# Kernel optimization log

Hardware: AMD Instinct MI355X
Metric: run time of the kernel (lower is better)

## Reference

```python
import jax, jax.numpy as jnp
import numpy as np

# TT-matrix embedding: vocab = 50*60*60 = 180000, embed_dim = 8*8*8 = 512, tt_rank = 16
M1, M2, M3 = 50, 60, 60        # row modes (index factorization)
N1, N2, N3 = 8, 8, 8           # col modes (embedding-dim factorization)
R = 16                         # TT rank
SENT, BATCH = 2048, 64
VOCAB = M1 * M2 * M3


def setup_inputs() -> dict:
    key = jax.random.key(0)
    k1, k2, k3, kx = jax.random.split(key, 4)
    scale = 0.3  # per-core stddev (t3.random_matrix uses a similar per-core normal init)
    # core k stored with the gathered (row-mode) axis first so gather is a plain take
    core1 = jax.random.normal(k1, (M1, N1, R), dtype=jnp.float32) * scale       # [m1, n1, r]
    core2 = jax.random.normal(k2, (M2, R, N2, R), dtype=jnp.float32) * scale    # [m2, r, n2, r]
    core3 = jax.random.normal(k3, (M3, R, N3), dtype=jnp.float32) * scale       # [m3, r, n3]
    x = jax.random.randint(kx, (SENT, BATCH), 0, VOCAB, dtype=jnp.int64)        # batch_dim_last=True layout
    return {"x": x, "core1": core1, "core2": core2, "core3": core3}


def reference(x, core1, core2, core3):
    # batch_dim_last=True: x is [sent, batch] -> permute to [batch, sent]
    sent, batch = x.shape
    flat = x.T.reshape(-1)                      # [T] flat token ids, T = batch*sent
    # t3.ind2sub: row-major mixed-radix decomposition over row modes [M1, M2, M3]
    i1 = flat // (M2 * M3)
    rem = flat % (M2 * M3)
    i2 = rem // M3
    i3 = rem % M3
    # gather one slice per TT core
    g1 = core1[i1]                              # [T, n1, r]
    g2 = core2[i2]                              # [T, r, n2, r]
    g3 = core3[i3]                              # [T, r, n3]
    # contract cores -> full embedding rows (t3.gather_rows(...).full())
    t12 = jnp.einsum('tar,trbs->tabs', g1, g2)  # [T, n1, n2, r]
    emb = jnp.einsum('tabs,tsc->tabc', t12, g3) # [T, n1, n2, n3]
    rows = emb.reshape(batch, sent, N1 * N2 * N3)
    # batch_dim_last=True: permute back to [sent, batch, emb_dim]
    return rows.transpose(1, 0, 2)
```

## Files before the change

kernel.cpp:

```cpp
#include <hip/hip_runtime.h>


#define M2M3 3600u
#define M3   60u
#define NPAIR 3000
#define CHUNK 16

__global__ __launch_bounds__(256) void tt_pair_kernel(
    const float* __restrict__ c1,
    const float* __restrict__ c2,
    float* __restrict__ tab)
{
    const int pair = blockIdx.x;
    const int i1 = pair / 60;
    const int i2 = pair - i1 * 60;
    const int tid = threadIdx.x;
    const int q  = tid >> 6;
    const int ab = tid & 63;
    const int a  = ab >> 3;
    const int b  = ab & 7;

    const float* __restrict__ g1 = c1 + i1 * 128 + a * 16;
    const float* __restrict__ g2 = c2 + i2 * 2048 + b * 16 + q * 4;

    float4 acc = make_float4(0.f, 0.f, 0.f, 0.f);
#pragma unroll
    for (int r = 0; r < 16; ++r) {
        const float a1 = g1[r];
        const float4 v = *(const float4*)(g2 + r * 128);
        acc.x = fmaf(a1, v.x, acc.x);
        acc.y = fmaf(a1, v.y, acc.y);
        acc.z = fmaf(a1, v.z, acc.z);
        acc.w = fmaf(a1, v.w, acc.w);
    }
    *(float4*)(tab + (size_t)pair * 1024 + tid * 4) = acc;
}

__global__ __launch_bounds__(256) void tt_zero_counts(unsigned* __restrict__ counts)
{
    const int i = blockIdx.x * blockDim.x + threadIdx.x;
    if (i < NPAIR) counts[i] = 0u;
}

__global__ __launch_bounds__(256) void tt_hist(
    const int* __restrict__ x, unsigned* __restrict__ counts, int T)
{
    const int t = blockIdx.x * blockDim.x + threadIdx.x;
    if (t >= T) return;
    const unsigned id = (unsigned)x[t];
    atomicAdd(&counts[id / M3], 1u);
}

__global__ __launch_bounds__(1024) void tt_scan(
    const unsigned* __restrict__ counts, unsigned* __restrict__ cursor)
{
    __shared__ unsigned buf[1024];
    const int tid = threadIdx.x;
    const int b = tid * 3;
    unsigned c0 = 0, c1 = 0, c2 = 0;
    if (b     < NPAIR) c0 = counts[b];
    if (b + 1 < NPAIR) c1 = counts[b + 1];
    if (b + 2 < NPAIR) c2 = counts[b + 2];
    const unsigned local = c0 + c1 + c2;
    buf[tid] = local;
    __syncthreads();
    for (int off = 1; off < 1024; off <<= 1) {
        const unsigned v = (tid >= off) ? buf[tid - off] : 0u;
        __syncthreads();
        buf[tid] += v;
        __syncthreads();
    }
    const unsigned excl = buf[tid] - local;
    if (b     < NPAIR) cursor[b]     = excl;
    if (b + 1 < NPAIR) cursor[b + 1] = excl + c0;
    if (b + 2 < NPAIR) cursor[b + 2] = excl + c0 + c1;
}

__global__ __launch_bounds__(256) void tt_scatter(
    const int* __restrict__ x, unsigned* __restrict__ cursor,
    unsigned* __restrict__ recT, unsigned* __restrict__ recPI, int T)
{
    const int t = blockIdx.x * blockDim.x + threadIdx.x;
    if (t >= T) return;
    const unsigned id   = (unsigned)x[t];
    const unsigned pair = id / M3;
    const unsigned i3   = id - pair * M3;
    const unsigned pos  = atomicAdd(&cursor[pair], 1u);
    recT[pos]  = (unsigned)t;
    recPI[pos] = (pair << 6) | i3;
}

__global__ __launch_bounds__(256) void tt_embed_sorted(
    const unsigned* __restrict__ recT,
    const unsigned* __restrict__ recPI,
    const float* __restrict__ c3,
    const float* __restrict__ tab,
    float* __restrict__ out,
    int T)
{
    const int wid  = (int)((blockIdx.x * blockDim.x + threadIdx.x) >> 6);
    const int lane = threadIdx.x & 63;
    const int base = wid * CHUNK;
    if (base >= T) return;

    unsigned rT = 0u, rP = 0u;
    if (lane < CHUNK && base + lane < T) {
        rT = recT[base + lane];
        rP = recPI[base + lane];
    }

    const int n = min(CHUNK, T - base);
    float4 t4[4];
    int cur = -1;

    for (int j = 0; j < n; ++j) {
        const unsigned tt = __builtin_amdgcn_readlane(rT, j);
        const unsigned pi = __builtin_amdgcn_readlane(rP, j);
        const int      pair = (int)(pi >> 6);
        const unsigned i3   = pi & 63u;

        if (pair != cur) {
            cur = pair;
            const float* tp = tab + (size_t)pair * 1024u;
#pragma unroll
            for (int q = 0; q < 4; ++q)
                t4[q] = *(const float4*)(tp + q * 256 + lane * 4);
        }
        const float* tf = (const float*)t4;

        const float4* __restrict__ g3 = (const float4*)(c3 + i3 * 128u);

        float o[8];
#pragma unroll
        for (int c = 0; c < 8; ++c) o[c] = 0.f;
#pragma unroll
        for (int s = 0; s < 16; ++s) {
            const float ts = tf[s];
            const float4 w0 = g3[s * 2 + 0];
            const float4 w1 = g3[s * 2 + 1];
            o[0] = fmaf(ts, w0.x, o[0]);
            o[1] = fmaf(ts, w0.y, o[1]);
            o[2] = fmaf(ts, w0.z, o[2]);
            o[3] = fmaf(ts, w0.w, o[3]);
            o[4] = fmaf(ts, w1.x, o[4]);
            o[5] = fmaf(ts, w1.y, o[5]);
            o[6] = fmaf(ts, w1.z, o[6]);
            o[7] = fmaf(ts, w1.w, o[7]);
        }

        float4* dst = (float4*)(out + (size_t)tt * 512u + lane * 8);
        dst[0] = make_float4(o[0], o[1], o[2], o[3]);
        dst[1] = make_float4(o[4], o[5], o[6], o[7]);
    }
}

__global__ __launch_bounds__(256) void tt_embed2_kernel(
    const int* __restrict__ x, const float* __restrict__ c3,
    const float* __restrict__ tab, float* __restrict__ out, int T)
{
    const int u    = (int)((blockIdx.x * blockDim.x + threadIdx.x) >> 6);
    const int lane = threadIdx.x & 63;
    if (u >= T) return;
    const unsigned id  = __builtin_amdgcn_readfirstlane((unsigned)x[u]);
    const unsigned i1  = id / M2M3;
    const unsigned rem = id - i1 * M2M3;
    const unsigned i2  = rem / M3;
    const unsigned i3  = rem - i2 * M3;
    const float* tp = tab + (size_t)(i1 * 60u + i2) * 1024u;
    float4 t[4];
#pragma unroll
    for (int q = 0; q < 4; ++q)
        t[q] = *(const float4*)(tp + q * 256 + lane * 4);
    const float* tf = (const float*)t;
    const float4* __restrict__ g3 = (const float4*)(c3 + i3 * 128u);
    float o[8];
#pragma unroll
    for (int c = 0; c < 8; ++c) o[c] = 0.f;
#pragma unroll
    for (int s = 0; s < 16; ++s) {
        const float ts = tf[s];
        const float4 w0 = g3[s * 2 + 0];
        const float4 w1 = g3[s * 2 + 1];
        o[0]=fmaf(ts,w0.x,o[0]); o[1]=fmaf(ts,w0.y,o[1]);
        o[2]=fmaf(ts,w0.z,o[2]); o[3]=fmaf(ts,w0.w,o[3]);
        o[4]=fmaf(ts,w1.x,o[4]); o[5]=fmaf(ts,w1.y,o[5]);
        o[6]=fmaf(ts,w1.z,o[6]); o[7]=fmaf(ts,w1.w,o[7]);
    }
    float4* dst = (float4*)(out + (size_t)u * 512 + lane * 8);
    dst[0] = make_float4(o[0], o[1], o[2], o[3]);
    dst[1] = make_float4(o[4], o[5], o[6], o[7]);
}

__global__ __launch_bounds__(256) void tt_embed_kernel(
    const int* __restrict__ x, const float* __restrict__ c1,
    const float* __restrict__ c2, const float* __restrict__ c3,
    float* __restrict__ out, int T)
{
    const int u    = (int)((blockIdx.x * blockDim.x + threadIdx.x) >> 6);
    const int lane = threadIdx.x & 63;
    if (u >= T) return;
    const int a = lane >> 3, b = lane & 7;
    const unsigned id  = (unsigned)x[u];
    const unsigned i1  = id / M2M3;
    const unsigned rem = id - i1 * M2M3;
    const unsigned i2  = rem / M3;
    const unsigned i3  = rem - i2 * M3;
    const float4* g1 = (const float4*)(c1 + i1 * 128u + a * 16);
    const float*  g2 = c2 + i2 * 2048u + b * 16;
    const float4* g3 = (const float4*)(c3 + i3 * 128u);
    float4 a1v[4];
#pragma unroll
    for (int q = 0; q < 4; ++q) a1v[q] = g1[q];
    const float* a1f = (const float*)a1v;
    float t12[16];
#pragma unroll
    for (int s = 0; s < 16; ++s) t12[s] = 0.f;
#pragma unroll
    for (int r = 0; r < 16; ++r) {
        const float a1 = a1f[r];
        const float4* row = (const float4*)(g2 + r * 128);
#pragma unroll
        for (int q = 0; q < 4; ++q) {
            const float4 v = row[q];
            t12[q*4+0] = fmaf(a1, v.x, t12[q*4+0]);
            t12[q*4+1] = fmaf(a1, v.y, t12[q*4+1]);
            t12[q*4+2] = fmaf(a1, v.z, t12[q*4+2]);
            t12[q*4+3] = fmaf(a1, v.w, t12[q*4+3]);
        }
    }
    float o[8];
#pragma unroll
    for (int c = 0; c < 8; ++c) o[c] = 0.f;
#pragma unroll
    for (int s = 0; s < 16; ++s) {
        const float ts = t12[s];
        const float4 w0 = g3[s*2+0];
        const float4 w1 = g3[s*2+1];
        o[0]=fmaf(ts,w0.x,o[0]); o[1]=fmaf(ts,w0.y,o[1]);
        o[2]=fmaf(ts,w0.z,o[2]); o[3]=fmaf(ts,w0.w,o[3]);
        o[4]=fmaf(ts,w1.x,o[4]); o[5]=fmaf(ts,w1.y,o[5]);
        o[6]=fmaf(ts,w1.z,o[6]); o[7]=fmaf(ts,w1.w,o[7]);
    }
    float4* dst = (float4*)(out + (size_t)u * 512 + lane * 8);
    dst[0] = make_float4(o[0], o[1], o[2], o[3]);
    dst[1] = make_float4(o[4], o[5], o[6], o[7]);
}

extern "C" void kernel_launch(void* const* d_in, const int* in_sizes, int n_in,
                              void* d_out, int out_size, void* d_ws, size_t ws_size,
                              hipStream_t stream) {
    const int*   x  = (const int*)d_in[0];
    const float* c1 = (const float*)d_in[1];
    const float* c2 = (const float*)d_in[2];
    const float* c3 = (const float*)d_in[3];
    float* out = (float*)d_out;

    const int T = in_sizes[0];

    const size_t tab_bytes  = (size_t)NPAIR * 1024u * sizeof(float);
    const size_t off_counts = tab_bytes;
    const size_t off_cursor = off_counts + 12032;
    const size_t off_recT   = off_cursor + 12032;
    const size_t off_recPI  = off_recT + (size_t)T * 4u;
    const size_t need_sort  = off_recPI + (size_t)T * 4u;

    char* ws = (char*)d_ws;

    if (ws_size >= need_sort) {
        float*    tab    = (float*)ws;
        unsigned* counts = (unsigned*)(ws + off_counts);
        unsigned* cursor = (unsigned*)(ws + off_cursor);
        unsigned* recT   = (unsigned*)(ws + off_recT);
        unsigned* recPI  = (unsigned*)(ws + off_recPI);

        tt_pair_kernel<<<NPAIR, 256, 0, stream>>>(c1, c2, tab);
        tt_zero_counts<<<(NPAIR + 255) / 256, 256, 0, stream>>>(counts);
        tt_hist<<<(T + 255) / 256, 256, 0, stream>>>(x, counts, T);
        tt_scan<<<1, 1024, 0, stream>>>(counts, cursor);
        tt_scatter<<<(T + 255) / 256, 256, 0, stream>>>(x, cursor, recT, recPI, T);
        const int waves  = (T + CHUNK - 1) / CHUNK;
        const int blocks = (waves + 3) / 4;
        tt_embed_sorted<<<blocks, 256, 0, stream>>>(recT, recPI, c3, tab, out, T);
    } else if (ws_size >= tab_bytes) {
        float* tab = (float*)ws;
        tt_pair_kernel<<<NPAIR, 256, 0, stream>>>(c1, c2, tab);
        const int blocks = (T + 3) / 4;
        tt_embed2_kernel<<<blocks, 256, 0, stream>>>(x, c3, tab, out, T);
    } else {
        const int blocks = (T + 3) / 4;
        tt_embed_kernel<<<blocks, 256, 0, stream>>>(x, c1, c2, c3, out, T);
    }
}
```

Measured before the change: 328.3 us.

## Fuse pair-table build into per-pair grouped embed kernel, pack sort records

Removes the separate pair-table kernel and its 12 MB workspace table: each block now handles one (i1,i2) pair, computes the core1×core2 product in registers, and applies it to every token bucketed to that pair. The scatter now writes one packed record (token<<6|i3) instead of two arrays, so record traffic is halved. After the atomic scatter the cursor holds bucket ends, which the kernel uses with counts to find each bucket's start. The trade-off is load imbalance across pairs (about 44 tokens per pair spread over 4 waves), per-wave serial loops over tokens, and the assumption that t<<6 fits in 32 bits.

```diff
diff --git a/kernel.cpp b/kernel.cpp
--- a/kernel.cpp
+++ b/kernel.cpp
@@ -1,45 +1,15 @@
 #include <hip/hip_runtime.h>
 
 
-#define M2M3 3600u
-#define M3   60u
+#define M2M3  3600u
+#define M3    60u
 #define NPAIR 3000
-#define CHUNK 16
-
-__global__ __launch_bounds__(256) void tt_pair_kernel(
-    const float* __restrict__ c1,
-    const float* __restrict__ c2,
-    float* __restrict__ tab)
-{
-    const int pair = blockIdx.x;
-    const int i1 = pair / 60;
-    const int i2 = pair - i1 * 60;
-    const int tid = threadIdx.x;
-    const int q  = tid >> 6;
-    const int ab = tid & 63;
-    const int a  = ab >> 3;
-    const int b  = ab & 7;
-
-    const float* __restrict__ g1 = c1 + i1 * 128 + a * 16;
-    const float* __restrict__ g2 = c2 + i2 * 2048 + b * 16 + q * 4;
-
-    float4 acc = make_float4(0.f, 0.f, 0.f, 0.f);
-#pragma unroll
-    for (int r = 0; r < 16; ++r) {
-        const float a1 = g1[r];
-        const float4 v = *(const float4*)(g2 + r * 128);
-        acc.x = fmaf(a1, v.x, acc.x);
-        acc.y = fmaf(a1, v.y, acc.y);
-        acc.z = fmaf(a1, v.z, acc.z);
-        acc.w = fmaf(a1, v.w, acc.w);
-    }
-    *(float4*)(tab + (size_t)pair * 1024 + tid * 4) = acc;
-}
-
-__global__ __launch_bounds__(256) void tt_zero_counts(unsigned* __restrict__ counts)
+#define NPAIR_PAD 3072
+
+__global__ __launch_bounds__(256) void tt_zero(unsigned* __restrict__ counts)
 {
     const int i = blockIdx.x * blockDim.x + threadIdx.x;
-    if (i < NPAIR) counts[i] = 0u;
+    if (i < NPAIR_PAD) counts[i] = 0u;
 }
 
 __global__ __launch_bounds__(256) void tt_hist(
@@ -78,7 +48,7 @@
 
 __global__ __launch_bounds__(256) void tt_scatter(
     const int* __restrict__ x, unsigned* __restrict__ cursor,
-    unsigned* __restrict__ recT, unsigned* __restrict__ recPI, int T)
+    unsigned* __restrict__ rec, int T)
 {
     const int t = blockIdx.x * blockDim.x + threadIdx.x;
     if (t >= T) return;
@@ -86,72 +56,125 @@
     const unsigned pair = id / M3;
     const unsigned i3   = id - pair * M3;
     const unsigned pos  = atomicAdd(&cursor[pair], 1u);
-    recT[pos]  = (unsigned)t;
-    recPI[pos] = (pair << 6) | i3;
-}
-
-__global__ __launch_bounds__(256) void tt_embed_sorted(
-    const unsigned* __restrict__ recT,
-    const unsigned* __restrict__ recPI,
+    rec[pos] = ((unsigned)t << 6) | i3;
+}
+
+__global__ __launch_bounds__(256) void tt_embed_grouped(
+    const unsigned* __restrict__ rec,
+    const unsigned* __restrict__ counts,
+    const unsigned* __restrict__ cursor,
+    const float* __restrict__ c1,
+    const float* __restrict__ c2,
     const float* __restrict__ c3,
-    const float* __restrict__ tab,
-    float* __restrict__ out,
-    int T)
-{
-    const int wid  = (int)((blockIdx.x * blockDim.x + threadIdx.x) >> 6);
+    float* __restrict__ out)
+{
+    const int p    = blockIdx.x;
     const int lane = threadIdx.x & 63;
-    const int base = wid * CHUNK;
-    if (base >= T) return;
-
-    unsigned rT = 0u, rP = 0u;
-    if (lane < CHUNK && base + lane < T) {
-        rT = recT[base + lane];
-        rP = recPI[base + lane];
-    }
-
-    const int n = min(CHUNK, T - base);
+    const int w    = threadIdx.x >> 6;
+    const int a    = lane >> 3;
+    const int b    = lane & 7;
+
+    unsigned end = cursor[p];
+    unsigned cnt = counts[p];
+    end = __builtin_amdgcn_readfirstlane(end);
+    cnt = __builtin_amdgcn_readfirstlane(cnt);
+    const unsigned start = end - cnt;
+
+    const unsigned q = cnt >> 2, r = cnt & 3u;
+    const unsigned nw = q + ((unsigned)w < r ? 1u : 0u);
+    if (nw == 0) return;
+    const unsigned bw = start + (unsigned)w * q + min((unsigned)w, r);
+
+    const int i1 = p / 60;
+    const int i2 = p - i1 * 60;
+    const float4* __restrict__ g1v = (const float4*)(c1 + i1 * 128 + a * 16);
+    const float*  __restrict__ g2  = c2 + i2 * 2048 + b * 16;
+
+    float4 a1q[4];
+#pragma unroll
+    for (int k = 0; k < 4; ++k) a1q[k] = g1v[k];
+    const float* a1f = (const float*)a1q;
+
     float4 t4[4];
-    int cur = -1;
-
-    for (int j = 0; j < n; ++j) {
-        const unsigned tt = __builtin_amdgcn_readlane(rT, j);
-        const unsigned pi = __builtin_amdgcn_readlane(rP, j);
-        const int      pair = (int)(pi >> 6);
-        const unsigned i3   = pi & 63u;
-
-        if (pair != cur) {
-            cur = pair;
-            const float* tp = tab + (size_t)pair * 1024u;
-#pragma unroll
-            for (int q = 0; q < 4; ++q)
-                t4[q] = *(const float4*)(tp + q * 256 + lane * 4);
+#pragma unroll
+    for (int k = 0; k < 4; ++k) t4[k] = make_float4(0.f, 0.f, 0.f, 0.f);
+#pragma unroll
+    for (int rr = 0; rr < 16; ++rr) {
+        const float a1 = a1f[rr];
+        const float4* row = (const float4*)(g2 + rr * 128);
+#pragma unroll
+        for (int k = 0; k < 4; ++k) {
+            const float4 v = row[k];
+            t4[k].x = fmaf(a1, v.x, t4[k].x);
+            t4[k].y = fmaf(a1, v.y, t4[k].y);
+            t4[k].z = fmaf(a1, v.z, t4[k].z);
+            t4[k].w = fmaf(a1, v.w, t4[k].w);
         }
-        const float* tf = (const float*)t4;
-
-        const float4* __restrict__ g3 = (const float4*)(c3 + i3 * 128u);
-
-        float o[8];
-#pragma unroll
-        for (int c = 0; c < 8; ++c) o[c] = 0.f;
-#pragma unroll
-        for (int s = 0; s < 16; ++s) {
-            const float ts = tf[s];
-            const float4 w0 = g3[s * 2 + 0];
-            const float4 w1 = g3[s * 2 + 1];
-            o[0] = fmaf(ts, w0.x, o[0]);
-            o[1] = fmaf(ts, w0.y, o[1]);
-            o[2] = fmaf(ts, w0.z, o[2]);
-            o[3] = fmaf(ts, w0.w, o[3]);
-            o[4] = fmaf(ts, w1.x, o[4]);
-            o[5] = fmaf(ts, w1.y, o[5]);
-            o[6] = fmaf(ts, w1.z, o[6]);
-            o[7] = fmaf(ts, w1.w, o[7]);
+    }
+    const float* tf = (const float*)t4;
+
+    for (unsigned off = 0; off < nw; off += 64u) {
+        const unsigned m = min(64u, nw - off);
+        unsigned rj = 0u;
+        if ((unsigned)lane < m) rj = rec[bw + off + (unsigned)lane];
+
+        for (unsigned j = 0; j < m; ++j) {
+            const unsigned rv = __builtin_amdgcn_readlane(rj, (int)j);
+            const unsigned t  = rv >> 6;
+            const unsigned i3 = rv & 63u;
+
+            const float4* __restrict__ g3 = (const float4*)(c3 + i3 * 128u);
+
+            float o[8];
+#pragma unroll
+            for (int c = 0; c < 8; ++c) o[c] = 0.f;
+#pragma unroll
+            for (int s = 0; s < 16; ++s) {
+                const float ts = tf[s];
+                const float4 w0 = g3[s * 2 + 0];
+                const float4 w1 = g3[s * 2 + 1];
+                o[0] = fmaf(ts, w0.x, o[0]);
+                o[1] = fmaf(ts, w0.y, o[1]);
+                o[2] = fmaf(ts, w0.z, o[2]);
+                o[3] = fmaf(ts, w0.w, o[3]);
+                o[4] = fmaf(ts, w1.x, o[4]);
+                o[5] = fmaf(ts, w1.y, o[5]);
+                o[6] = fmaf(ts, w1.z, o[6]);
+                o[7] = fmaf(ts, w1.w, o[7]);
+            }
+
+            float4* dst = (float4*)(out + (size_t)t * 512u + lane * 8);
+            dst[0] = make_float4(o[0], o[1], o[2], o[3]);
+            dst[1] = make_float4(o[4], o[5], o[6], o[7]);
         }
-
-        float4* dst = (float4*)(out + (size_t)tt * 512u + lane * 8);
-        dst[0] = make_float4(o[0], o[1], o[2], o[3]);
-        dst[1] = make_float4(o[4], o[5], o[6], o[7]);
-    }
+    }
+}
+
+__global__ __launch_bounds__(256) void tt_pair_kernel(
+    const float* __restrict__ c1, const float* __restrict__ c2,
+    float* __restrict__ tab)
+{
+    const int pair = blockIdx.x;
+    const int i1 = pair / 60;
+    const int i2 = pair - i1 * 60;
+    const int tid = threadIdx.x;
+    const int qq = tid >> 6;
+    const int ab = tid & 63;
+    const int a  = ab >> 3;
+    const int b  = ab & 7;
+    const float* __restrict__ g1 = c1 + i1 * 128 + a * 16;
+    const float* __restrict__ g2 = c2 + i2 * 2048 + b * 16 + qq * 4;
+    float4 acc = make_float4(0.f, 0.f, 0.f, 0.f);
+#pragma unroll
+    for (int rr = 0; rr < 16; ++rr) {
+        const float a1 = g1[rr];
+        const float4 v = *(const float4*)(g2 + rr * 128);
+        acc.x = fmaf(a1, v.x, acc.x);
+        acc.y = fmaf(a1, v.y, acc.y);
+        acc.z = fmaf(a1, v.z, acc.z);
+        acc.w = fmaf(a1, v.w, acc.w);
+    }
+    *(float4*)(tab + (size_t)pair * 1024 + tid * 4) = acc;
 }
 
 __global__ __launch_bounds__(256) void tt_embed2_kernel(
@@ -169,8 +192,8 @@
     const float* tp = tab + (size_t)(i1 * 60u + i2) * 1024u;
     float4 t[4];
 #pragma unroll
-    for (int q = 0; q < 4; ++q)
-        t[q] = *(const float4*)(tp + q * 256 + lane * 4);
+    for (int k = 0; k < 4; ++k)
+        t[k] = *(const float4*)(tp + k * 256 + lane * 4);
     const float* tf = (const float*)t;
     const float4* __restrict__ g3 = (const float4*)(c3 + i3 * 128u);
     float o[8];
@@ -210,22 +233,22 @@
     const float4* g3 = (const float4*)(c3 + i3 * 128u);
     float4 a1v[4];
 #pragma unroll
-    for (int q = 0; q < 4; ++q) a1v[q] = g1[q];
+    for (int k = 0; k < 4; ++k) a1v[k] = g1[k];
     const float* a1f = (const float*)a1v;
     float t12[16];
 #pragma unroll
     for (int s = 0; s < 16; ++s) t12[s] = 0.f;
 #pragma unroll
-    for (int r = 0; r < 16; ++r) {
-        const float a1 = a1f[r];
-        const float4* row = (const float4*)(g2 + r * 128);
-#pragma unroll
-        for (int q = 0; q < 4; ++q) {
-            const float4 v = row[q];
-            t12[q*4+0] = fmaf(a1, v.x, t12[q*4+0]);
-            t12[q*4+1] = fmaf(a1, v.y, t12[q*4+1]);
-            t12[q*4+2] = fmaf(a1, v.z, t12[q*4+2]);
-            t12[q*4+3] = fmaf(a1, v.w, t12[q*4+3]);
+    for (int rr = 0; rr < 16; ++rr) {
+        const float a1 = a1f[rr];
+        const float4* row = (const float4*)(g2 + rr * 128);
+#pragma unroll
+        for (int k = 0; k < 4; ++k) {
+            const float4 v = row[k];
+            t12[k*4+0] = fmaf(a1, v.x, t12[k*4+0]);
+            t12[k*4+1] = fmaf(a1, v.y, t12[k*4+1]);
+            t12[k*4+2] = fmaf(a1, v.z, t12[k*4+2]);
+            t12[k*4+3] = fmaf(a1, v.w, t12[k*4+3]);
         }
     }
     float o[8];
@@ -257,30 +280,25 @@
 
     const int T = in_sizes[0];
 
+    const size_t off_counts = 0;
+    const size_t off_cursor = off_counts + (size_t)NPAIR_PAD * 4u;
+    const size_t off_rec    = off_cursor + (size_t)NPAIR_PAD * 4u;
+    const size_t need_sort  = off_rec + (size_t)T * 4u;
     const size_t tab_bytes  = (size_t)NPAIR * 1024u * sizeof(float);
-    const size_t off_counts = tab_bytes;
-    const size_t off_cursor = off_counts + 12032;
-    const size_t off_recT   = off_cursor + 12032;
-    const size_t off_recPI  = off_recT + (size_t)T * 4u;
-    const size_t need_sort  = off_recPI + (size_t)T * 4u;
 
     char* ws = (char*)d_ws;
 
     if (ws_size >= need_sort) {
-        float*    tab    = (float*)ws;
         unsigned* counts = (unsigned*)(ws + off_counts);
         unsigned* cursor = (unsigned*)(ws + off_cursor);
-        unsigned* recT   = (unsigned*)(ws + off_recT);
-        unsigned* recPI  = (unsigned*)(ws + off_recPI);
-
-        tt_pair_kernel<<<NPAIR, 256, 0, stream>>>(c1, c2, tab);
-        tt_zero_counts<<<(NPAIR + 255) / 256, 256, 0, stream>>>(counts);
+        unsigned* rec    = (unsigned*)(ws + off_rec);
+
+        tt_zero<<<(NPAIR_PAD + 255) / 256, 256, 0, stream>>>(counts);
         tt_hist<<<(T + 255) / 256, 256, 0, stream>>>(x, counts, T);
         tt_scan<<<1, 1024, 0, stream>>>(counts, cursor);
-        tt_scatter<<<(T + 255) / 256, 256, 0, stream>>>(x, cursor, recT, recPI, T);
-        const int waves  = (T + CHUNK - 1) / CHUNK;
-        const int blocks = (waves + 3) / 4;
-        tt_embed_sorted<<<blocks, 256, 0, stream>>>(recT, recPI, c3, tab, out, T);
+        tt_scatter<<<(T + 255) / 256, 256, 0, stream>>>(x, cursor, rec, T);
+        tt_embed_grouped<<<NPAIR, 256, 0, stream>>>(rec, counts, cursor,
+                                                    c1, c2, c3, out);
     } else if (ws_size >= tab_bytes) {
         float* tab = (float*)ws;
         tt_pair_kernel<<<NPAIR, 256, 0, stream>>>(c1, c2, tab);
```

Result: no change. 324.2 us (-1.3%).
